# Performance work log

Hardware: AMD Instinct MI355X
Metric: run time of the kernel (lower is better)

## Reference

```python
import jax, jax.numpy as jnp
import numpy as np

B, N, Q, Z, C, L = 1, 6, 20000, 4, 128, 4
IMG_H, IMG_W = 256, 704
PC_RANGE = (-50.0, -50.0, -4.0, 50.0, 50.0, 4.0)
NUM_FREQS = 10
EPS = 1e-5
LEVEL_HW = ((64, 176), (32, 88), (16, 44), (8, 22))


def _mlp(x, ws, bs):
    for i, (w, b) in enumerate(zip(ws, bs)):
        x = x @ w + b
        if i < len(ws) - 1:
            x = jax.nn.relu(x)
    return x


def _bilinear(feat_hwc, px, py):
    # feat_hwc: [H, W, C]; px, py: [P] pixel coords. align_corners=False, zero padding.
    H, W, _ = feat_hwc.shape
    x0 = jnp.floor(px).astype(jnp.int32)
    y0 = jnp.floor(py).astype(jnp.int32)
    wx = px - x0
    wy = py - y0

    def gather(yi, xi):
        inb = ((yi >= 0) & (yi < H) & (xi >= 0) & (xi < W)).astype(feat_hwc.dtype)
        return feat_hwc[jnp.clip(yi, 0, H - 1), jnp.clip(xi, 0, W - 1)] * inb[:, None]

    return (gather(y0, x0) * ((1 - wy) * (1 - wx))[:, None]
          + gather(y0, x0 + 1) * ((1 - wy) * wx)[:, None]
          + gather(y0 + 1, x0) * (wy * (1 - wx))[:, None]
          + gather(y0 + 1, x0 + 1) * (wy * wx)[:, None])


def _pointbev_forward(feats, reference_points, lidar2img,
                      pe_w1, pe_b1, pe_w2, pe_b2, wt_w, wt_b, hm_ws, hm_bs):
    pos = jnp.transpose(reference_points, (0, 2, 1, 3))            # [B,Q,Z,3] in [0,1]
    # sinusoidal positional encoding map (normalized=False: coords used as-is)
    freqs = (2.0 ** jnp.arange(NUM_FREQS, dtype=pos.dtype)) * jnp.pi
    ang = pos[..., None] * freqs                                   # [B,Q,Z,3,F]
    pe_in = jnp.concatenate([jnp.sin(ang), jnp.cos(ang)], axis=-1)
    pe_in = pe_in.reshape(pos.shape[:-1] + (3 * 2 * NUM_FREQS,))
    pos_emb = _mlp(pe_in, [pe_w1, pe_w2], [pe_b1, pe_b2])          # [B,Q,Z,C]
    scale_w = jax.nn.softmax(pos_emb @ wt_w + wt_b, axis=-1)       # [B,Q,Z,L]

    # unnormalize to metric lidar coords via pc_range
    lo = jnp.asarray(PC_RANGE[:3], pos.dtype)
    span = jnp.asarray(PC_RANGE[3:], pos.dtype) - lo
    pts4 = jnp.concatenate([pos * span + lo, jnp.ones_like(pos[..., :1])], axis=-1)
    cam = jnp.einsum('bnij,bqzj->bnqzi', lidar2img, pts4)          # [B,N,Q,Z,4]
    homo = cam[..., 2]
    uv = cam[..., :2] / jnp.maximum(homo, EPS)[..., None]
    u = uv[..., 0] / IMG_W
    v = uv[..., 1] / IMG_H
    valid = ((homo > EPS) & (u > 0.0) & (u < 1.0) & (v > 0.0) & (v < 1.0)).astype(pos.dtype)

    sampler = jax.vmap(_bilinear)
    uf = u.reshape(B * N, Q * Z)
    vf = v.reshape(B * N, Q * Z)
    out = jnp.zeros((B, Q, Z, C), pos.dtype)
    for l, feat in enumerate(feats):                               # L=4 fixed levels
        Hl, Wl = feat.shape[2], feat.shape[3]
        s = sampler(feat.reshape(B * N, Hl, Wl, C), uf * Wl - 0.5, vf * Hl - 0.5)
        s = s.reshape(B, N, Q, Z, C) * valid[..., None]            # mask invalid projections
        out = out + s.sum(axis=1) * scale_w[..., l, None]          # sum views, weight level
    out = (out + pos_emb).reshape(B, Q, Z * C)
    return _mlp(out, hm_ws, hm_bs)                                 # [B,Q,C]


def setup_inputs():
    key = jax.random.key(0)
    ks = jax.random.split(key, 32)
    inp = {}
    for l, (h, w) in enumerate(LEVEL_HW):
        inp[f"feat{l}"] = jax.random.normal(ks[l], (B, N, h, w, C), jnp.float32)
    inp["reference_points"] = jax.random.uniform(ks[8], (B, Z, Q, 3), jnp.float32)
    # structured nuScenes-like lidar2img = intrinsics @ extrinsics for a 6-camera ring
    l2i = np.zeros((B, N, 4, 4), np.float32)
    K = np.array([[400.0, 0.0, IMG_W / 2, 0.0],
                  [0.0, 400.0, IMG_H / 2, 0.0],
                  [0.0, 0.0, 1.0, 0.0],
                  [0.0, 0.0, 0.0, 1.0]], np.float32)
    for n in range(N):
        yaw = 2.0 * np.pi * n / N
        cy, sy = np.cos(yaw), np.sin(yaw)
        R = np.array([[-sy, cy, 0.0], [0.0, 0.0, -1.0], [cy, sy, 0.0]], np.float32)
        E = np.eye(4, dtype=np.float32)
        E[:3, :3] = R
        E[:3, 3] = [0.0, 1.5, 0.5]
        l2i[0, n] = K @ E
    inp["lidar2img"] = jnp.asarray(l2i)

    def lin(k, fi, fo):
        s = 1.0 / np.sqrt(fi)
        return jax.random.uniform(k, (fi, fo), jnp.float32, -s, s)

    d_in = 3 * 2 * NUM_FREQS
    inp["pe_w1"] = lin(ks[9], d_in, 2 * C); inp["pe_b1"] = jnp.zeros((2 * C,), jnp.float32)
    inp["pe_w2"] = lin(ks[10], 2 * C, C);   inp["pe_b2"] = jnp.zeros((C,), jnp.float32)
    inp["wt_w"] = lin(ks[11], C, L);        inp["wt_b"] = jnp.zeros((L,), jnp.float32)
    dims = [Z * C, 2 * Z * C, 2 * Z * C, 2 * Z * C, C]
    for i in range(4):
        inp[f"hm_w{i+1}"] = lin(ks[12 + i], dims[i], dims[i + 1])
        inp[f"hm_b{i+1}"] = jnp.zeros((dims[i + 1],), jnp.float32)
    return inp


def reference(feat0, feat1, feat2, feat3, reference_points, lidar2img,
              pe_w1, pe_b1, pe_w2, pe_b2, wt_w, wt_b,
              hm_w1, hm_b1, hm_w2, hm_b2, hm_w3, hm_b3, hm_w4, hm_b4):
    return _pointbev_forward((feat0, feat1, feat2, feat3), reference_points, lidar2img,
                             pe_w1, pe_b1, pe_w2, pe_b2, wt_w, wt_b,
                             [hm_w1, hm_w2, hm_w3, hm_w4], [hm_b1, hm_b2, hm_b3, hm_b4])
```

## Files before the change

kernel.cpp:

```cpp
#include <hip/hip_runtime.h>
#include <math.h>

#define QN 20000
#define PN 80000
#define CN 128
#define NVIEW 6

typedef __attribute__((ext_vector_type(8))) _Float16 h8;
typedef __attribute__((ext_vector_type(4))) _Float16 h4;
typedef __attribute__((ext_vector_type(4))) float f32x4;

__device__ __forceinline__ void gload16(const void* g, void* l) {
  __builtin_amdgcn_global_load_lds(
      (const __attribute__((address_space(1))) void*)g,
      (__attribute__((address_space(3))) void*)l, 16, 0, 0);
}

__global__ __launch_bounds__(256) void prep_all(
    const float* __restrict__ w0, const float* __restrict__ w1,
    const float* __restrict__ w2, const float* __restrict__ w3,
    const float* __restrict__ w4, const float* __restrict__ w5,
    _Float16* __restrict__ wbase,
    const float* __restrict__ s0, const float* __restrict__ s1,
    const float* __restrict__ s2, const float* __restrict__ s3,
    _Float16* __restrict__ fdst,
    const float* __restrict__ rp, _Float16* __restrict__ pedst) {
  int b = blockIdx.x;
  if (b < 2736) {
    __shared__ float t[32][33];
    const float* W; _Float16* T; int K, N, Kp, nbx, lb;
    if (b < 16)        { W = w0; T = wbase + 0;       K = 60;   N = 256;  Kp = 64;   nbx = 8;  lb = b; }
    else if (b < 48)   { W = w1; T = wbase + 32768;   K = 256;  N = 128;  Kp = 256;  nbx = 4;  lb = b - 16; }
    else if (b < 560)  { W = w2; T = wbase + 98304;   K = 512;  N = 1024; Kp = 512;  nbx = 32; lb = b - 48; }
    else if (b < 1584) { W = w3; T = wbase + 1146880; K = 1024; N = 1024; Kp = 1024; nbx = 32; lb = b - 560; }
    else if (b < 2608) { W = w4; T = wbase + 3244032; K = 1024; N = 1024; Kp = 1024; nbx = 32; lb = b - 1584; }
    else               { W = w5; T = wbase + 5341184; K = 1024; N = 128;  Kp = 1024; nbx = 4;  lb = b - 2608; }
    const int n0 = (lb % nbx) * 32, k0 = (lb / nbx) * 32;
    const int tx = threadIdx.x & 31, ty = threadIdx.x >> 5;
    #pragma unroll
    for (int j = 0; j < 4; ++j) {
      int k = k0 + ty + j * 8;
      t[ty + j * 8][tx] = (k < K) ? W[(size_t)k * N + n0 + tx] : 0.f;
    }
    __syncthreads();
    #pragma unroll
    for (int j = 0; j < 4; ++j) {
      int n = n0 + ty + j * 8;
      int k = k0 + tx;
      T[(size_t)n * Kp + k] = (_Float16)t[tx][ty + j * 8];
    }
  } else if (b < 13956) {
    size_t i = (size_t)(b - 2736) * 256 + threadIdx.x;
    const float* s; size_t off;
    if (i < 2162688)      { s = s0; off = 0; }
    else if (i < 2703360) { s = s1; off = 2162688; }
    else if (i < 2838528) { s = s2; off = 2703360; }
    else                  { s = s3; off = 2838528; }
    f32x4 v = *(const f32x4*)(s + (i - off) * 4);
    h4 o;
    o[0] = (_Float16)v[0]; o[1] = (_Float16)v[1];
    o[2] = (_Float16)v[2]; o[3] = (_Float16)v[3];
    *(h4*)(fdst + i * 4) = o;
  } else {
    int idx = (b - 13956) * 256 + threadIdx.x;
    int p = idx >> 6, k = idx & 63;
    float val = 0.f;
    if (k < 60) {
      int q = p >> 2, z = p & 3;
      int d = k / 20, r = k - d * 20;
      int j = (r >= 10) ? (r - 10) : r;
      float pos = rp[((size_t)z * QN + q) * 3 + d];
      float ang = pos * ((float)(1 << j) * 3.14159265358979323846f);
      val = (r >= 10) ? cosf(ang) : sinf(ang);
    }
    pedst[idx] = (_Float16)val;
  }
}

__global__ __launch_bounds__(256) void lw_kernel(const _Float16* __restrict__ posE,
                                                 const float* __restrict__ wtw,
                                                 const float* __restrict__ wtb,
                                                 float* __restrict__ lw) {
  __shared__ float swtT[512];
  __shared__ float sb[4];
  const int tid = threadIdx.x;
  for (int i = tid; i < 512; i += 256) swtT[(i & 3) * 128 + (i >> 2)] = wtw[i];
  if (tid < 4) sb[tid] = wtb[tid];
  __syncthreads();

  const int wave = tid >> 6, lane = tid & 63;
  const int grp = lane >> 4, s = lane & 15;
  const int p = blockIdx.x * 16 + wave * 4 + grp;
  const int c0 = s * 8;
  h8 pa = *(const h8*)(posE + (size_t)p * CN + c0);

  float lg[4];
  #pragma unroll
  for (int l = 0; l < 4; ++l) {
    const float* w = swtT + l * 128 + c0;
    float acc = 0.f;
    #pragma unroll
    for (int j = 0; j < 8; ++j) acc = fmaf((float)pa[j], w[j], acc);
    lg[l] = acc;
  }
  #pragma unroll
  for (int off = 8; off > 0; off >>= 1) {
    lg[0] += __shfl_xor(lg[0], off);
    lg[1] += __shfl_xor(lg[1], off);
    lg[2] += __shfl_xor(lg[2], off);
    lg[3] += __shfl_xor(lg[3], off);
  }
  lg[0] += sb[0]; lg[1] += sb[1]; lg[2] += sb[2]; lg[3] += sb[3];
  float mx = fmaxf(fmaxf(lg[0], lg[1]), fmaxf(lg[2], lg[3]));
  float e0 = __expf(lg[0] - mx), e1 = __expf(lg[1] - mx);
  float e2 = __expf(lg[2] - mx), e3 = __expf(lg[3] - mx);
  float esr = 1.f / (e0 + e1 + e2 + e3);
  if (s == 0) {
    f32x4 o = {e0 * esr, e1 * esr, e2 * esr, e3 * esr};
    *(f32x4*)(lw + (size_t)p * 4) = o;
  }
}

template <bool RELU, int OUT>
__global__ __launch_bounds__(256, 4) void gemm_h(const _Float16* __restrict__ A,
                                                 const _Float16* __restrict__ B,
                                                 const float* __restrict__ bias,
                                                 float* __restrict__ Cf,
                                                 _Float16* __restrict__ Ch,
                                                 int M, int N, int K,
                                                 int nbn) {
  __shared__ _Float16 sm[2][2][4096];
  const int tid = threadIdx.x;
  const int wave = tid >> 6, lane = tid & 63;
  const int wr = wave >> 1, wc = wave & 1;
  const int g = lane >> 4, r16 = lane & 15;

  const int nwg = gridDim.x;
  const int q8 = nwg >> 3, r8 = nwg & 7;
  const int xcd = blockIdx.x & 7, sub = blockIdx.x >> 3;
  const int wg = (xcd < r8 ? xcd * (q8 + 1) : r8 * (q8 + 1) + (xcd - r8) * q8) + sub;
  const int bn = (wg % nbn) * 128;
  const int bm = (wg / nbn) * 128;
  const int nt = K >> 5;

  f32x4 acc[4][4];
  #pragma unroll
  for (int i = 0; i < 4; ++i)
    #pragma unroll
    for (int j = 0; j < 4; ++j) acc[i][j] = {0.f, 0.f, 0.f, 0.f};

  auto STAGE = [&](int buf, int t) {
    const int kof = t << 5;
    const int rsub = lane >> 2;
    const int slot0 = lane & 3;
    #pragma unroll
    for (int pl = 0; pl < 2; ++pl) {
      const _Float16* P = (pl == 0) ? A : B;
      const int rbase = (pl == 0) ? bm : bn;
      #pragma unroll
      for (int i = 0; i < 2; ++i) {
        int group = wave * 2 + i;
        int row = group * 16 + rsub;
        int slot = slot0 ^ ((row >> 1) & 3);
        int gr = rbase + row;
        if (pl == 0 && gr >= M) gr = M - 1;
        gload16(P + (size_t)gr * K + kof + slot * 8,
                &sm[buf][pl][group * 512]);
      }
    }
  };

  auto COMPUTE = [&](int buf) {
    h8 a[4], b[4];
    #pragma unroll
    for (int mi = 0; mi < 4; ++mi) {
      int row = wr * 64 + mi * 16 + r16;
      int off = row * 32 + ((g ^ ((row >> 1) & 3)) * 8);
      a[mi] = *(const h8*)&sm[buf][0][off];
    }
    #pragma unroll
    for (int ni = 0; ni < 4; ++ni) {
      int row = wc * 64 + ni * 16 + r16;
      int off = row * 32 + ((g ^ ((row >> 1) & 3)) * 8);
      b[ni] = *(const h8*)&sm[buf][1][off];
    }
    #pragma unroll
    for (int mi = 0; mi < 4; ++mi)
      #pragma unroll
      for (int ni = 0; ni < 4; ++ni)
        acc[mi][ni] = __builtin_amdgcn_mfma_f32_16x16x32_f16(a[mi], b[ni], acc[mi][ni], 0, 0, 0);
  };

  STAGE(0, 0);
  __syncthreads();

  for (int t = 0; t < nt; ++t) {
    if (t + 1 < nt) STAGE((t + 1) & 1, t + 1);
    COMPUTE(t & 1);
    __syncthreads();
  }

  #pragma unroll
  for (int mi = 0; mi < 4; ++mi) {
    int gr0 = bm + wr * 64 + mi * 16 + (lane >> 4) * 4;
    #pragma unroll
    for (int ni = 0; ni < 4; ++ni) {
      int gc = bn + wc * 64 + ni * 16 + r16;
      float bv = bias[gc];
      #pragma unroll
      for (int r = 0; r < 4; ++r) {
        int row = gr0 + r;
        if (row >= M) continue;
        float v = acc[mi][ni][r] + bv;
        if (RELU) v = fmaxf(v, 0.f);
        if (OUT == 0) Cf[(size_t)row * N + gc] = v;
        else          Ch[(size_t)row * N + gc] = (_Float16)v;
      }
    }
  }
}

__global__ __launch_bounds__(256) void sample_kernel(
    const _Float16* __restrict__ fbase,
    const float* __restrict__ rp, const float* __restrict__ l2i,
    const float* __restrict__ lw,
    const _Float16* __restrict__ posE, _Float16* __restrict__ X0) {
  __shared__ float sl2i[96];
  const int tid = threadIdx.x;
  if (tid < 96) sl2i[tid] = l2i[tid];
  __syncthreads();

  const _Float16* FL[4] = {fbase, fbase + 8650752, fbase + 10813440,
                           fbase + 11354112};

  const int wave = tid >> 6, lane = tid & 63;
  const int half = lane >> 5, s = lane & 31;
  const int p = blockIdx.x * 8 + wave * 2 + half;
  const int q = p >> 2, z = p & 3;

  const float X  = rp[((size_t)z * QN + q) * 3 + 0] * 100.f - 50.f;
  const float Y  = rp[((size_t)z * QN + q) * 3 + 1] * 100.f - 50.f;
  const float Zc = rp[((size_t)z * QN + q) * 3 + 2] * 8.f - 4.f;

  const int c0 = s * 4;
  h4 pa = *(const h4*)(posE + (size_t)p * CN + c0);
  const float pe0 = (float)pa[0], pe1 = (float)pa[1];
  const float pe2 = (float)pa[2], pe3 = (float)pa[3];

  f32x4 lw4 = *(const f32x4*)(lw + (size_t)p * 4);
  float swl[4] = {lw4[0], lw4[1], lw4[2], lw4[3]};

  float a0 = 0.f, a1 = 0.f, a2 = 0.f, a3 = 0.f;
  for (int n = 0; n < NVIEW; n++) {
    const float* Mx = sl2i + n * 16;
    float cam0 = Mx[0] * X + Mx[1] * Y + Mx[2]  * Zc + Mx[3];
    float cam1 = Mx[4] * X + Mx[5] * Y + Mx[6]  * Zc + Mx[7];
    float cam2 = Mx[8] * X + Mx[9] * Y + Mx[10] * Zc + Mx[11];
    float denom = fmaxf(cam2, 1e-5f);
    float u = cam0 / denom * (1.f / 704.f);
    float v = cam1 / denom * (1.f / 256.f);
    bool valid = (cam2 > 1e-5f) & (u > 0.f) & (u < 1.f) & (v > 0.f) & (v < 1.f);
    if (!valid) continue;
    float px3 = u * 22.f - 0.5f, py3 = v * 8.f - 0.5f;
    bool interior = (px3 >= 0.f) & (py3 >= 0.f) & (px3 < 21.f) & (py3 < 7.f);
    if (interior) {
      #pragma unroll
      for (int l = 0; l < 4; l++) {
        const int Hl = 64 >> l, Wl = 176 >> l;
        float pxl = u * (float)Wl - 0.5f;
        float pyl = v * (float)Hl - 0.5f;
        float fx = floorf(pxl), fy = floorf(pyl);
        int x0 = (int)fx, y0 = (int)fy;
        float wx = pxl - fx, wy = pyl - fy;
        float w1r = wy * swl[l], w0r = swl[l] - w1r;
        float w01 = w0r * wx, w00 = w0r - w01;
        float w11 = w1r * wx, w10 = w1r - w11;
        const _Float16* cp = FL[l]
            + ((size_t)n * (Hl * Wl) + (size_t)(y0 * Wl + x0)) * CN + c0;
        h4 v00 = *(const h4*)(cp);
        h4 v01 = *(const h4*)(cp + CN);
        h4 v10 = *(const h4*)(cp + Wl * CN);
        h4 v11 = *(const h4*)(cp + Wl * CN + CN);
        a0 = fmaf(w00, (float)v00[0], fmaf(w01, (float)v01[0], fmaf(w10, (float)v10[0], fmaf(w11, (float)v11[0], a0))));
        a1 = fmaf(w00, (float)v00[1], fmaf(w01, (float)v01[1], fmaf(w10, (float)v10[1], fmaf(w11, (float)v11[1], a1))));
        a2 = fmaf(w00, (float)v00[2], fmaf(w01, (float)v01[2], fmaf(w10, (float)v10[2], fmaf(w11, (float)v11[2], a2))));
        a3 = fmaf(w00, (float)v00[3], fmaf(w01, (float)v01[3], fmaf(w10, (float)v10[3], fmaf(w11, (float)v11[3], a3))));
      }
    } else {
      #pragma unroll
      for (int l = 0; l < 4; l++) {
        const int Hl = 64 >> l, Wl = 176 >> l;
        float pxl = u * (float)Wl - 0.5f;
        float pyl = v * (float)Hl - 0.5f;
        float fx = floorf(pxl), fy = floorf(pyl);
        int x0 = (int)fx, y0 = (int)fy;
        float wx = pxl - fx, wy = pyl - fy;
        float w1r = wy * swl[l], w0r = swl[l] - w1r;
        const float wxs[2] = {1.f - wx, wx};
        const float wrs[2] = {w0r, w1r};
        const _Float16* fb = FL[l] + (size_t)n * (Hl * Wl) * CN;
        #pragma unroll
        for (int cy = 0; cy < 2; cy++) {
          #pragma unroll
          for (int cx = 0; cx < 2; cx++) {
            int xi = x0 + cx, yi = y0 + cy;
            bool inb = ((unsigned)xi < (unsigned)Wl) & ((unsigned)yi < (unsigned)Hl);
            int off = inb ? (yi * Wl + xi) * CN : 0;
            float wgt = inb ? (wrs[cy] * wxs[cx]) : 0.f;
            h4 vv = *(const h4*)(fb + off + c0);
            a0 = fmaf(wgt, (float)vv[0], a0);
            a1 = fmaf(wgt, (float)vv[1], a1);
            a2 = fmaf(wgt, (float)vv[2], a2);
            a3 = fmaf(wgt, (float)vv[3], a3);
          }
        }
      }
    }
  }
  h4 o;
  o[0] = (_Float16)(a0 + pe0);
  o[1] = (_Float16)(a1 + pe1);
  o[2] = (_Float16)(a2 + pe2);
  o[3] = (_Float16)(a3 + pe3);
  *(h4*)&X0[(size_t)p * CN + c0] = o;
}

extern "C" void kernel_launch(void* const* d_in, const int* in_sizes, int n_in,
                              void* d_out, int out_size, void* d_ws, size_t ws_size,
                              hipStream_t stream) {
  const float* feat0 = (const float*)d_in[0];
  const float* feat1 = (const float*)d_in[1];
  const float* feat2 = (const float*)d_in[2];
  const float* feat3 = (const float*)d_in[3];
  const float* rp    = (const float*)d_in[4];
  const float* l2i   = (const float*)d_in[5];
  const float* pe_w1 = (const float*)d_in[6];
  const float* pe_b1 = (const float*)d_in[7];
  const float* pe_w2 = (const float*)d_in[8];
  const float* pe_b2 = (const float*)d_in[9];
  const float* wt_w  = (const float*)d_in[10];
  const float* wt_b  = (const float*)d_in[11];
  const float* hm_w1 = (const float*)d_in[12];
  const float* hm_b1 = (const float*)d_in[13];
  const float* hm_w2 = (const float*)d_in[14];
  const float* hm_b2 = (const float*)d_in[15];
  const float* hm_w3 = (const float*)d_in[16];
  const float* hm_b3 = (const float*)d_in[17];
  const float* hm_w4 = (const float*)d_in[18];
  const float* hm_b4 = (const float*)d_in[19];
  float* out = (float*)d_out;

  char* ws = (char*)d_ws;
  typedef _Float16 h16;
  h16* wPE1 = (h16*)(ws + 0);
  h16* wPE2 = (h16*)(ws + 65536);
  h16* wH1  = (h16*)(ws + 196608);
  h16* wH2  = (h16*)(ws + 2293760);
  h16* wH3  = (h16*)(ws + 6488064);
  h16* wH4  = (h16*)(ws + 10682368);

  h16*   posE = (h16*)(ws + 11534336);
  float* lwga = (float*)(ws + 33000000);
  h16*   hpe  = (h16*)(ws + 53000192);
  h16*   pein = (h16*)(ws + 94000128);
  h16*   X0   = (h16*)(ws + 53000192);
  h16*   H1   = (h16*)(ws + 94000128);
  h16*   H2   = (h16*)(ws + 11534336);
  h16*   H3   = (h16*)(ws + 94000128);
  h16*   f16b = (h16*)(ws + 136000000);

  prep_all<<<33956, 256, 0, stream>>>(pe_w1, pe_w2, hm_w1, hm_w2, hm_w3, hm_w4,
                                      (h16*)ws, feat0, feat1, feat2, feat3,
                                      f16b, rp, pein);

  gemm_h<true, 1><<<2 * 625, 256, 0, stream>>>(pein, wPE1, pe_b1, nullptr, hpe, PN, 256, 64, 2);
  gemm_h<false, 1><<<1 * 625, 256, 0, stream>>>(hpe, wPE2, pe_b2, nullptr, posE, PN, 128, 256, 1);

  lw_kernel<<<PN / 16, 256, 0, stream>>>(posE, wt_w, wt_b, lwga);

  sample_kernel<<<PN / 8, 256, 0, stream>>>(f16b, rp, l2i, lwga, posE, X0);

  gemm_h<true, 1><<<8 * 157, 256, 0, stream>>>(X0, wH1, hm_b1, nullptr, H1, QN, 1024, 512, 8);
  gemm_h<true, 1><<<8 * 157, 256, 0, stream>>>(H1, wH2, hm_b2, nullptr, H2, QN, 1024, 1024, 8);
  gemm_h<true, 1><<<8 * 157, 256, 0, stream>>>(H2, wH3, hm_b3, nullptr, H3, QN, 1024, 1024, 8);
  gemm_h<false, 0><<<1 * 157, 256, 0, stream>>>(H3, wH4, hm_b4, out, nullptr, QN, 128, 1024, 1);
}
```

Baseline: 314.3 us.

## Widen GEMM K-tile to 64 and replace double buffering with single-buffered staging

The GEMM K-step goes from 32 to 64, with a new 8-slot XOR swizzle over a 128x64 LDS tile for A and B. The double-buffered prefetch is replaced by a single buffer with a stage, sync, compute, sync loop. This halves the number of loop iterations and barriers per tile. In exchange, global-to-LDS loads no longer overlap MFMA compute, and the first GEMM with K=64 becomes a single iteration.

```diff
diff --git a/kernel.cpp b/kernel.cpp
--- a/kernel.cpp
+++ b/kernel.cpp
@@ -122,14 +122,15 @@
 }
 
 template <bool RELU, int OUT>
-__global__ __launch_bounds__(256, 4) void gemm_h(const _Float16* __restrict__ A,
+__global__ __launch_bounds__(256, 4) void gemm97(const _Float16* __restrict__ A,
                                                  const _Float16* __restrict__ B,
                                                  const float* __restrict__ bias,
                                                  float* __restrict__ Cf,
                                                  _Float16* __restrict__ Ch,
                                                  int M, int N, int K,
                                                  int nbn) {
-  __shared__ _Float16 sm[2][2][4096];
+  __shared__ _Float16 smA[128 * 64];
+  __shared__ _Float16 smB[128 * 64];
   const int tid = threadIdx.x;
   const int wave = tid >> 6, lane = tid & 63;
   const int wr = wave >> 1, wc = wave & 1;
@@ -141,7 +142,7 @@
   const int wg = (xcd < r8 ? xcd * (q8 + 1) : r8 * (q8 + 1) + (xcd - r8) * q8) + sub;
   const int bn = (wg % nbn) * 128;
   const int bm = (wg / nbn) * 128;
-  const int nt = K >> 5;
+  const int nt = K >> 6;
 
   f32x4 acc[4][4];
   #pragma unroll
@@ -149,54 +150,56 @@
     #pragma unroll
     for (int j = 0; j < 4; ++j) acc[i][j] = {0.f, 0.f, 0.f, 0.f};
 
-  auto STAGE = [&](int buf, int t) {
-    const int kof = t << 5;
-    const int rsub = lane >> 2;
-    const int slot0 = lane & 3;
+  auto STAGE = [&](int t) {
+    const int kof = t << 6;
+    const int rsub = lane >> 3;
+    const int slot0 = lane & 7;
     #pragma unroll
     for (int pl = 0; pl < 2; ++pl) {
       const _Float16* P = (pl == 0) ? A : B;
+      _Float16* S = (pl == 0) ? smA : smB;
       const int rbase = (pl == 0) ? bm : bn;
       #pragma unroll
-      for (int i = 0; i < 2; ++i) {
-        int group = wave * 2 + i;
-        int row = group * 16 + rsub;
-        int slot = slot0 ^ ((row >> 1) & 3);
+      for (int i = 0; i < 4; ++i) {
+        int group = wave * 4 + i;
+        int row = group * 8 + rsub;
+        int slot = slot0 ^ (row & 7);
         int gr = rbase + row;
         if (pl == 0 && gr >= M) gr = M - 1;
         gload16(P + (size_t)gr * K + kof + slot * 8,
-                &sm[buf][pl][group * 512]);
+                &S[group * 512]);
       }
     }
   };
 
-  auto COMPUTE = [&](int buf) {
-    h8 a[4], b[4];
-    #pragma unroll
-    for (int mi = 0; mi < 4; ++mi) {
-      int row = wr * 64 + mi * 16 + r16;
-      int off = row * 32 + ((g ^ ((row >> 1) & 3)) * 8);
-      a[mi] = *(const h8*)&sm[buf][0][off];
-    }
-    #pragma unroll
-    for (int ni = 0; ni < 4; ++ni) {
-      int row = wc * 64 + ni * 16 + r16;
-      int off = row * 32 + ((g ^ ((row >> 1) & 3)) * 8);
-      b[ni] = *(const h8*)&sm[buf][1][off];
-    }
-    #pragma unroll
-    for (int mi = 0; mi < 4; ++mi)
-      #pragma unroll
-      for (int ni = 0; ni < 4; ++ni)
-        acc[mi][ni] = __builtin_amdgcn_mfma_f32_16x16x32_f16(a[mi], b[ni], acc[mi][ni], 0, 0, 0);
+  auto COMPUTE = [&]() {
+    #pragma unroll
+    for (int kk = 0; kk < 2; ++kk) {
+      h8 a[4], b[4];
+      #pragma unroll
+      for (int mi = 0; mi < 4; ++mi) {
+        int row = wr * 64 + mi * 16 + r16;
+        int off = row * 64 + (((kk * 4 + g) ^ (row & 7)) * 8);
+        a[mi] = *(const h8*)&smA[off];
+      }
+      #pragma unroll
+      for (int ni = 0; ni < 4; ++ni) {
+        int row = wc * 64 + ni * 16 + r16;
+        int off = row * 64 + (((kk * 4 + g) ^ (row & 7)) * 8);
+        b[ni] = *(const h8*)&smB[off];
+      }
+      #pragma unroll
+      for (int mi = 0; mi < 4; ++mi)
+        #pragma unroll
+        for (int ni = 0; ni < 4; ++ni)
+          acc[mi][ni] = __builtin_amdgcn_mfma_f32_16x16x32_f16(a[mi], b[ni], acc[mi][ni], 0, 0, 0);
+    }
   };
 
-  STAGE(0, 0);
-  __syncthreads();
-
   for (int t = 0; t < nt; ++t) {
-    if (t + 1 < nt) STAGE((t + 1) & 1, t + 1);
-    COMPUTE(t & 1);
+    STAGE(t);
+    __syncthreads();
+    COMPUTE();
     __syncthreads();
   }
 
@@ -373,15 +376,15 @@
                                       (h16*)ws, feat0, feat1, feat2, feat3,
                                       f16b, rp, pein);
 
-  gemm_h<true, 1><<<2 * 625, 256, 0, stream>>>(pein, wPE1, pe_b1, nullptr, hpe, PN, 256, 64, 2);
-  gemm_h<false, 1><<<1 * 625, 256, 0, stream>>>(hpe, wPE2, pe_b2, nullptr, posE, PN, 128, 256, 1);
+  gemm97<true, 1><<<2 * 625, 256, 0, stream>>>(pein, wPE1, pe_b1, nullptr, hpe, PN, 256, 64, 2);
+  gemm97<false, 1><<<1 * 625, 256, 0, stream>>>(hpe, wPE2, pe_b2, nullptr, posE, PN, 128, 256, 1);
 
   lw_kernel<<<PN / 16, 256, 0, stream>>>(posE, wt_w, wt_b, lwga);
 
   sample_kernel<<<PN / 8, 256, 0, stream>>>(f16b, rp, l2i, lwga, posE, X0);
 
-  gemm_h<true, 1><<<8 * 157, 256, 0, stream>>>(X0, wH1, hm_b1, nullptr, H1, QN, 1024, 512, 8);
-  gemm_h<true, 1><<<8 * 157, 256, 0, stream>>>(H1, wH2, hm_b2, nullptr, H2, QN, 1024, 1024, 8);
-  gemm_h<true, 1><<<8 * 157, 256, 0, stream>>>(H2, wH3, hm_b3, nullptr, H3, QN, 1024, 1024, 8);
-  gemm_h<false, 0><<<1 * 157, 256, 0, stream>>>(H3, wH4, hm_b4, out, nullptr, QN, 128, 1024, 1);
-}
+  gemm97<true, 1><<<8 * 157, 256, 0, stream>>>(X0, wH1, hm_b1, nullptr, H1, QN, 1024, 512, 8);
+  gemm97<true, 1><<<8 * 157, 256, 0, stream>>>(H1, wH2, hm_b2, nullptr, H2, QN, 1024, 1024, 8);
+  gemm97<true, 1><<<8 * 157, 256, 0, stream>>>(H2, wH3, hm_b3, nullptr, H3, QN, 1024, 1024, 8);
+  gemm97<false, 0><<<1 * 157, 256, 0, stream>>>(H3, wH4, hm_b4, out, nullptr, QN, 128, 1024, 1);
+}
```

After: 304.6 us. -3.1%, faster.
